# Kernel optimization log

Hardware: AMD Instinct MI355X
Metric: run time of the kernel (lower is better)

Reference implementation:

```python
import jax, jax.numpy as jnp
import numpy as np

D = 768
H = 12
HD = D // H
FF = 3072
EPS = 1e-5


def layernorm(x, g, b):
    mu = jnp.mean(x, axis=-1, keepdims=True)
    var = jnp.mean(jnp.square(x - mu), axis=-1, keepdims=True)
    return (x - mu) * jax.lax.rsqrt(var + EPS) * g + b


def setup_inputs() -> dict:
    key = jax.random.key(0)
    ks = jax.random.split(key, 12)
    s = 0.02
    return {
        "x": jax.random.normal(ks[0], (4, 1024, D), dtype=jnp.float32),
        "w_qkv": jax.random.normal(ks[1], (D, 3 * D), dtype=jnp.float32) * s,
        "b_qkv": jnp.zeros((3 * D,), jnp.float32),
        "w_proj": jax.random.normal(ks[2], (D, D), dtype=jnp.float32) * s,
        "b_proj": jnp.zeros((D,), jnp.float32),
        "w1": jax.random.normal(ks[3], (D, FF), dtype=jnp.float32) * s,
        "b1": jnp.zeros((FF,), jnp.float32),
        "w2": jax.random.normal(ks[4], (FF, D), dtype=jnp.float32) * s,
        "b2": jnp.zeros((D,), jnp.float32),
        "g1": jnp.ones((D,), jnp.float32),
        "be1": jnp.zeros((D,), jnp.float32),
        "g2": jnp.ones((D,), jnp.float32),
        "be2": jnp.zeros((D,), jnp.float32),
    }


def reference(x, w_qkv, b_qkv, w_proj, b_proj, w1, b1, w2, b2, g1, be1, g2, be2):
    B, N, C = x.shape
    # --- attention (pre-norm) ---
    h = layernorm(x, g1, be1)
    qkv = (h @ w_qkv + b_qkv).reshape(B, N, 3, H, HD)
    q = jnp.transpose(qkv[:, :, 0], (0, 2, 1, 3))  # [B,H,N,hd]
    k = jnp.transpose(qkv[:, :, 1], (0, 2, 1, 3))
    v = jnp.transpose(qkv[:, :, 2], (0, 2, 1, 3))
    attn = jnp.einsum("bhqd,bhkd->bhqk", q, k) * (HD ** -0.5)
    attn = jax.nn.softmax(attn, axis=-1)
    o = jnp.einsum("bhqk,bhkd->bhqd", attn, v)
    o = jnp.transpose(o, (0, 2, 1, 3)).reshape(B, N, C)
    x = x + (o @ w_proj + b_proj)
    # --- feedforward (pre-norm) ---
    h2 = layernorm(x, g2, be2)
    ff = jax.nn.gelu(h2 @ w1 + b1, approximate=False) @ w2 + b2
    return x + ff
```

## Files before the change

### kernel.cpp

```cpp
#include <hip/hip_runtime.h>
#include <hip/hip_bf16.h>
#include <math.h>

typedef __attribute__((ext_vector_type(8))) short short8;
typedef __attribute__((ext_vector_type(4))) float f32x4;

#define DMODEL 768
#define THREE_D 2304
#define FFDIM 3072
#define NSEQ 1024
#define NHEAD 12
#define HEADD 64
#define MROWS 4096

__device__ __forceinline__ ushort f2bf(float f) {
  union { float f; unsigned u; } c; c.f = f;
  unsigned u = c.u;
  unsigned r = (u + 0x7fffu + ((u >> 16) & 1u)) >> 16;
  return (ushort)r;
}

__device__ __forceinline__ float bf2f(ushort u) {
  union { float f; unsigned u; } c; c.u = ((unsigned)u) << 16; return c.f;
}

__device__ __forceinline__ unsigned pack2bf(float a, float b) {
  union { __hip_bfloat162 h; unsigned u; } c;
  c.h = __float22bfloat162_rn(make_float2(a, b));
  return c.u;
}

__device__ __forceinline__ void load_lds16(const ushort* g, const ushort* l) {
  __builtin_amdgcn_global_load_lds(
      (const __attribute__((address_space(1))) unsigned int*)g,
      (__attribute__((address_space(3))) unsigned int*)l, 16, 0, 0);
}

template <int N> __device__ __forceinline__ void wait_vm() {
  if constexpr (N == 8)      asm volatile("s_waitcnt vmcnt(8)" ::: "memory");
  else if constexpr (N == 6) asm volatile("s_waitcnt vmcnt(6)" ::: "memory");
  else if constexpr (N == 4) asm volatile("s_waitcnt vmcnt(4)" ::: "memory");
  else                       asm volatile("s_waitcnt vmcnt(0)" ::: "memory");
}

__device__ __forceinline__ void ln_body(const float* __restrict__ x,
    const float* __restrict__ g, const float* __restrict__ be,
    ushort* __restrict__ out, int row, int tid,
    float* red1, float* red2) {
  const float* xr = x + (size_t)row * DMODEL;
  float v0 = xr[tid], v1 = xr[tid + 256], v2 = xr[tid + 512];
  float s = v0 + v1 + v2;
  #pragma unroll
  for (int off = 32; off; off >>= 1) s += __shfl_xor(s, off);
  if ((tid & 63) == 0) red1[tid >> 6] = s;
  __syncthreads();
  float mean = (red1[0] + red1[1] + red1[2] + red1[3]) * (1.0f / 768.0f);
  float d0 = v0 - mean, d1 = v1 - mean, d2 = v2 - mean;
  float q = d0 * d0 + d1 * d1 + d2 * d2;
  #pragma unroll
  for (int off = 32; off; off >>= 1) q += __shfl_xor(q, off);
  if ((tid & 63) == 0) red2[tid >> 6] = q;
  __syncthreads();
  float var = (red2[0] + red2[1] + red2[2] + red2[3]) * (1.0f / 768.0f);
  float rs = rsqrtf(var + 1e-5f);
  size_t base = (size_t)row * DMODEL;
  out[base + tid]       = f2bf(d0 * rs * g[tid]       + be[tid]);
  out[base + tid + 256] = f2bf(d1 * rs * g[tid + 256] + be[tid + 256]);
  out[base + tid + 512] = f2bf(d2 * rs * g[tid + 512] + be[tid + 512]);
}

__global__ __launch_bounds__(256) void ln_bf16_kernel(
    const ushort* __restrict__ x, const float* __restrict__ g,
    const float* __restrict__ be, ushort* __restrict__ out) {
  __shared__ float red1[4], red2[4];
  int row = blockIdx.x, tid = threadIdx.x;
  const ushort* xr = x + (size_t)row * DMODEL;
  float v0 = 0.f, v1 = 0.f, v2 = 0.f, v3 = 0.f;
  if (tid < 192) {
    ushort4 u = *(const ushort4*)&xr[tid * 4];
    v0 = bf2f(u.x); v1 = bf2f(u.y); v2 = bf2f(u.z); v3 = bf2f(u.w);
  }
  float s = v0 + v1 + v2 + v3;
  #pragma unroll
  for (int off = 32; off; off >>= 1) s += __shfl_xor(s, off);
  if ((tid & 63) == 0) red1[tid >> 6] = s;
  __syncthreads();
  float mean = (red1[0] + red1[1] + red1[2] + red1[3]) * (1.0f / 768.0f);
  float d0 = v0 - mean, d1 = v1 - mean, d2 = v2 - mean, d3 = v3 - mean;
  float q = (tid < 192) ? d0 * d0 + d1 * d1 + d2 * d2 + d3 * d3 : 0.f;
  #pragma unroll
  for (int off = 32; off; off >>= 1) q += __shfl_xor(q, off);
  if ((tid & 63) == 0) red2[tid >> 6] = q;
  __syncthreads();
  float var = (red2[0] + red2[1] + red2[2] + red2[3]) * (1.0f / 768.0f);
  float rs = rsqrtf(var + 1e-5f);
  if (tid < 192) {
    int c = tid * 4;
    float o0 = d0 * rs * g[c] + be[c];
    float o1 = d1 * rs * g[c + 1] + be[c + 1];
    float o2 = d2 * rs * g[c + 2] + be[c + 2];
    float o3 = d3 * rs * g[c + 3] + be[c + 3];
    uint2 pw = make_uint2(pack2bf(o0, o1), pack2bf(o2, o3));
    *(uint2*)&out[(size_t)row * DMODEL + c] = pw;
  }
}

__global__ __launch_bounds__(256) void pre_kernel(
    const float* __restrict__ w_qkv, const float* __restrict__ w_proj,
    const float* __restrict__ w1, const float* __restrict__ w2,
    ushort* __restrict__ Wqkv_t, ushort* __restrict__ Wproj_t,
    ushort* __restrict__ W1_t, ushort* __restrict__ W2_t,
    const float* __restrict__ x, const float* __restrict__ g1,
    const float* __restrict__ be1, ushort* __restrict__ hbuf) {
  __shared__ float t[64][33];
  int id = blockIdx.x;
  int tid = threadIdx.x;
  if (id >= 3456) {
    ln_body(x, g1, be1, hbuf, id - 3456, tid, &t[0][0], &t[1][0]);
    return;
  }
  const float* W; ushort* Wt; int K, N, bx, by;
  if (id < 864)       { W = w_qkv;  Wt = Wqkv_t;  K = 768;  N = 2304; bx = id % 72; by = id / 72; }
  else if (id < 1152) { id -= 864;  W = w_proj; Wt = Wproj_t; K = 768;  N = 768;  bx = id % 24; by = id / 24; }
  else if (id < 2304) { id -= 1152; W = w1;     Wt = W1_t;    K = 768;  N = 3072; bx = id % 96; by = id / 96; }
  else                { id -= 2304; W = w2;     Wt = W2_t;    K = 3072; N = 768;  bx = id % 24; by = id / 24; }
  int n0 = bx * 32, k0 = by * 64;
  #pragma unroll
  for (int i = 0; i < 2; i++) {
    int s = tid + i * 256;
    int k = s >> 3, nq = (s & 7) * 4;
    float4 w = *(const float4*)&W[(size_t)(k0 + k) * N + n0 + nq];
    t[k][nq] = w.x; t[k][nq + 1] = w.y; t[k][nq + 2] = w.z; t[k][nq + 3] = w.w;
  }
  __syncthreads();
  {
    int n = tid >> 3, kq = (tid & 7) * 8;
    ushort u[8];
    #pragma unroll
    for (int j = 0; j < 8; j++) u[j] = f2bf(t[kq + j][n]);
    *(int4*)&Wt[(size_t)(n0 + n) * K + k0 + kq] = *(int4*)u;
  }
}

__global__ void vt_kernel(const ushort* __restrict__ qkv, ushort* __restrict__ Vt) {
  __shared__ ushort t[32][33];
  int n0 = blockIdx.x * 32, d0 = blockIdx.y * 32, bh = blockIdx.z;
  int b = bh / NHEAD, hh = bh % NHEAD;
  int tx = threadIdx.x, ty = threadIdx.y;
  #pragma unroll
  for (int r = 0; r < 4; r++)
    t[ty + r * 8][tx] = qkv[(size_t)(b * NSEQ + n0 + ty + r * 8) * THREE_D +
                            2 * DMODEL + hh * HEADD + d0 + tx];
  __syncthreads();
  #pragma unroll
  for (int r = 0; r < 4; r++) {
    int n = n0 + tx;
    int np = (n & ~63) | (((n & 15) << 2) | ((n >> 4) & 3));
    Vt[((size_t)bh * HEADD + d0 + ty + r * 8) * NSEQ + np] = t[tx][ty + r * 8];
  }
}

template <int BN, int MODE>
__global__ __launch_bounds__(512, 2) void gemm256_kernel(
    const ushort* __restrict__ A, const ushort* __restrict__ Bt,
    const float* __restrict__ bias, void* __restrict__ Cout,
    int gx, int Ntot, int K) {
  constexpr int FN = BN / 64;
  constexpr int WN = BN / 4;
  constexpr int ABUF = (256 + BN) * 64;
  constexpr int BOFF = 256 * 64;
  __shared__ ushort S[2 * ABUF];
  int tid = threadIdx.x, lane = tid & 63, wave = tid >> 6;
  int wm = wave >> 2, wn = wave & 3;
  int rsel = lane & 15, quad = lane >> 4;
  int nwg = gridDim.x;
  int o = blockIdx.x;
  int wg = (o & 7) * (nwg >> 3) + (o >> 3);
  int bx = wg % gx, by = wg / gx;
  int m0 = by * 256, n0 = bx * BN;
  f32x4 acc[8][FN] = {};
  int xorc = (rsel & 7) * 8;

  auto SA = [&](int buf, int k0, int i) {
    int c0 = i * 512 + wave * 64;
    int c = c0 + lane, r = c >> 3;
    int kk = ((c ^ r) & 7) * 8;
    load_lds16(&A[(size_t)(m0 + r) * K + k0 + kk], S + buf * ABUF + c0 * 8);
  };
  auto SB = [&](int buf, int k0, int i) {
    int c0 = i * 512 + wave * 64;
    int c = c0 + lane, r = c >> 3;
    int kk = ((c ^ r) & 7) * 8;
    load_lds16(&Bt[(size_t)(n0 + r) * K + k0 + kk],
               S + buf * ABUF + BOFF + c0 * 8);
  };
  auto RDA = [&](int cur, int half, int ks, int mi) -> short8 {
    int R = wm * 128 + (half * 4 + mi) * 16 + rsel;
    return *(const short8*)&S[cur * ABUF + R * 64 + ((ks * 32 + quad * 8) ^ xorc)];
  };
  auto RDB = [&](int cur, int ks, int ni) -> short8 {
    int R = wn * WN + ni * 16 + rsel;
    return *(const short8*)&S[cur * ABUF + BOFF + R * 64 +
                              ((ks * 32 + quad * 8) ^ xorc)];
  };

  #pragma unroll
  for (int i = 0; i < 4; i++) SA(0, 0, i);
  #pragma unroll
  for (int i = 0; i < FN; i++) SB(0, 0, i);
  wait_vm<0>();
  __builtin_amdgcn_s_barrier();

  int ntk = K >> 6;
  for (int t = 0; t < ntk; t++) {
    int cur = t & 1, nxt = cur ^ 1;
    bool pre = (t + 1 < ntk);
    int nk0 = (t + 1) * 64;
    short8 afb[2][4], bfb[2][FN];
    #pragma unroll
    for (int mi = 0; mi < 4; mi++) afb[0][mi] = RDA(cur, 0, 0, mi);
    #pragma unroll
    for (int ni = 0; ni < FN; ni++) bfb[0][ni] = RDB(cur, 0, ni);
    #pragma unroll
    for (int p = 0; p < 4; p++) {
      const int ks = p >> 1, half = p & 1;
      if (p < 3) {
        const int ksn = (p + 1) >> 1, halfn = (p + 1) & 1;
        #pragma unroll
        for (int mi = 0; mi < 4; mi++)
          afb[(p + 1) & 1][mi] = RDA(cur, halfn, ksn, mi);
        if (p == 1) {
          #pragma unroll
          for (int ni = 0; ni < FN; ni++) bfb[1][ni] = RDB(cur, 1, ni);
        }
      }
      if (pre) {
        if (p == 0) {
          #pragma unroll
          for (int i = 0; i < FN; i++) SB(nxt, nk0, i);
          SA(nxt, nk0, 0);
        } else if (p == 1) {
          SA(nxt, nk0, 1); SA(nxt, nk0, 2); SA(nxt, nk0, 3);
        }
      }
      __builtin_amdgcn_s_setprio(1);
      #pragma unroll
      for (int mi = 0; mi < 4; mi++)
        #pragma unroll
        for (int ni = 0; ni < FN; ni++)
          acc[half * 4 + mi][ni] = __builtin_amdgcn_mfma_f32_16x16x32_bf16(
              afb[p & 1][mi], bfb[ks][ni], acc[half * 4 + mi][ni], 0, 0, 0);
      __builtin_amdgcn_s_setprio(0);
    }
    wait_vm<0>();
    __builtin_amdgcn_s_barrier();
  }
  ushort* Cl = S;
  float bv[FN];
  #pragma unroll
  for (int ni = 0; ni < FN; ni++) bv[ni] = bias[n0 + wn * WN + ni * 16 + rsel];
  #pragma unroll
  for (int mi = 0; mi < 8; mi++) {
    int row = wm * 128 + mi * 16 + quad * 4;
    #pragma unroll
    for (int ni = 0; ni < FN; ni++) {
      int col = wn * WN + ni * 16 + rsel;
      #pragma unroll
      for (int j = 0; j < 4; j++) {
        float v = acc[mi][ni][j] + bv[ni];
        if (MODE == 2) v = 0.5f * v * (1.0f + erff(v * 0.70710678118654752f));
        Cl[(row + j) * 200 + col] = f2bf(v);
      }
    }
  }
  __syncthreads();
  constexpr int CPR = BN / 8;
  ushort* Cg = (ushort*)Cout;
  for (int c = tid; c < 256 * CPR; c += 512) {
    int row = c / CPR, off = c - row * CPR;
    int4 v = *(const int4*)&Cl[row * 200 + off * 8];
    *(int4*)&Cg[(size_t)(m0 + row) * Ntot + n0 + off * 8] = v;
  }
}

template <int BM, int BN, int MODE>
__global__ __launch_bounds__(256) void gemm_kernel(
    const ushort* __restrict__ A, const ushort* __restrict__ Bt,
    const float* __restrict__ bias, const void* __restrict__ resid,
    void* __restrict__ Cout, int gx, int Ntot, int K) {
  constexpr int ABUF = (BM + BN) * 64;
  constexpr int BOFF = BM * 64;
  constexpr int CSTR = BN + 4;
  constexpr int SMEM = (2 * ABUF * 2 > BM * CSTR * 4) ? 2 * ABUF
                                                      : BM * CSTR * 2;
  __shared__ ushort S[SMEM];
  constexpr int WM = BM / 2, WN = BN / 2;
  constexpr int FM = WM / 16, FN = WN / 16;
  constexpr int NL = BM / 32 + BN / 32;
  int tid = threadIdx.x, lane = tid & 63, wave = tid >> 6;
  int wm = wave >> 1, wn = wave & 1;
  int rsel = lane & 15, quad = lane >> 4;
  int nwg = gridDim.x;
  int o = blockIdx.x;
  int wg = (o & 7) * (nwg >> 3) + (o >> 3);
  int bx = wg % gx, by = wg / gx;
  int m0 = by * BM, n0 = bx * BN;
  f32x4 acc[FM][FN] = {};

  auto STAGE = [&](int buf, int k0) {
    #pragma unroll
    for (int i = 0; i < BM / 32; i++) {
      int c0 = i * 256 + wave * 64;
      int c = c0 + lane, r = c >> 3;
      int kk = ((c ^ r) & 7) * 8;
      load_lds16(&A[(size_t)(m0 + r) * K + k0 + kk], S + buf * ABUF + c0 * 8);
    }
    #pragma unroll
    for (int i = 0; i < BN / 32; i++) {
      int c0 = i * 256 + wave * 64;
      int c = c0 + lane, r = c >> 3;
      int kk = ((c ^ r) & 7) * 8;
      load_lds16(&Bt[(size_t)(n0 + r) * K + k0 + kk],
                 S + buf * ABUF + BOFF + c0 * 8);
    }
  };

  STAGE(0, 0);
  int ntk = K >> 6;
  for (int t = 0; t < ntk; t++) {
    int cur = t & 1;
    if (t + 1 < ntk) {
      STAGE(cur ^ 1, (t + 1) * 64);
      wait_vm<NL>();
    } else {
      wait_vm<0>();
    }
    __builtin_amdgcn_s_barrier();
    short8 af[2][FM], bf[2][FN];
    #pragma unroll
    for (int ks = 0; ks < 2; ks++) {
      int ko = ks * 32 + quad * 8;
      #pragma unroll
      for (int mi = 0; mi < FM; mi++) {
        int R = wm * WM + mi * 16 + rsel;
        af[ks][mi] = *(const short8*)&S[cur * ABUF + R * 64 + (ko ^ ((R & 7) * 8))];
      }
      #pragma unroll
      for (int ni = 0; ni < FN; ni++) {
        int R = wn * WN + ni * 16 + rsel;
        bf[ks][ni] = *(const short8*)&S[cur * ABUF + BOFF + R * 64 + (ko ^ ((R & 7) * 8))];
      }
    }
    #pragma unroll
    for (int ks = 0; ks < 2; ks++)
      #pragma unroll
      for (int mi = 0; mi < FM; mi++)
        #pragma unroll
        for (int ni = 0; ni < FN; ni++)
          acc[mi][ni] = __builtin_amdgcn_mfma_f32_16x16x32_bf16(
              af[ks][mi], bf[ks][ni], acc[mi][ni], 0, 0, 0);
    asm volatile("s_waitcnt lgkmcnt(0)" ::: "memory");
    __builtin_amdgcn_s_barrier();
  }
  float* Cl = (float*)S;
  #pragma unroll
  for (int ni = 0; ni < FN; ni++) {
    int col = wn * WN + ni * 16 + rsel;
    float bvv = bias[n0 + col];
    #pragma unroll
    for (int mi = 0; mi < FM; mi++) {
      int row = wm * WM + mi * 16 + quad * 4;
      #pragma unroll
      for (int j = 0; j < 4; j++)
        Cl[(row + j) * CSTR + col] = acc[mi][ni][j] + bvv;
    }
  }
  __syncthreads();
  constexpr int CPR = BN / 4;
  for (int c = tid; c < BM * CPR; c += 256) {
    int row = c / CPR, off = c - row * CPR;
    size_t gi = (size_t)(m0 + row) * Ntot + n0 + off * 4;
    float4 v = *(const float4*)&Cl[row * CSTR + off * 4];
    if (MODE == 0) {
      float4 rr = *(const float4*)&((const float*)resid)[gi];
      v.x += rr.x; v.y += rr.y; v.z += rr.z; v.w += rr.w;
      uint2 pw = make_uint2(pack2bf(v.x, v.y), pack2bf(v.z, v.w));
      *(uint2*)&((ushort*)Cout)[gi] = pw;
    } else {
      ushort4 rr = *(const ushort4*)&((const ushort*)resid)[gi];
      v.x += bf2f(rr.x); v.y += bf2f(rr.y);
      v.z += bf2f(rr.z); v.w += bf2f(rr.w);
      *(float4*)&((float*)Cout)[gi] = v;
    }
  }
}

__global__ __launch_bounds__(512) void attn_kernel(
    const ushort* __restrict__ qkv, const ushort* __restrict__ Vt,
    ushort* __restrict__ o) {
  __shared__ ushort Klds[2][64][64];
  __shared__ ushort Vlds[2][64][64];
  __shared__ ushort Plds[8][16][72];
  const float CL2 = 0.18033688011112042f;
  int tid = threadIdx.x, lane = tid & 63, wave = tid >> 6;
  int id = blockIdx.x;
  int qt = id / 48, bh = id % 48;
  int b = bh / NHEAD, hh = bh % NHEAD;
  int q0 = qt * 128;
  int rsel = lane & 15, quad = lane >> 4;
  int xorc = (rsel & 7) * 8;

  short8 qf[2];
  {
    int qrow = q0 + wave * 16 + rsel;
    const ushort* qp = qkv + (size_t)(b * NSEQ + qrow) * THREE_D + hh * HEADD + quad * 8;
    qf[0] = *(const short8*)qp;
    qf[1] = *(const short8*)(qp + 32);
  }
  short8 onesf;
  #pragma unroll
  for (int i = 0; i < 8; i++) onesf[i] = (short)0x3F80;

  int r0 = tid >> 3, d0 = (tid & 7) * 8;
  int sw0 = d0 ^ ((r0 & 7) * 8);
  const ushort* Kg = qkv + (size_t)b * NSEQ * THREE_D + DMODEL + hh * HEADD;
  const ushort* Vg = Vt + (size_t)bh * HEADD * NSEQ;
  int4 kr0, vr0;
  auto LD = [&](int kv0) {
    kr0 = *(const int4*)&Kg[(size_t)(kv0 + r0) * THREE_D + d0];
    vr0 = *(const int4*)&Vg[(size_t)r0 * NSEQ + kv0 + d0];
  };
  auto ST = [&](int bf) {
    *(int4*)&Klds[bf][r0][sw0] = kr0;
    *(int4*)&Vlds[bf][r0][sw0] = vr0;
  };

  f32x4 oacc[4] = {};
  f32x4 osum = {};

  LD(0); ST(0); __syncthreads();

  for (int t = 0; t < 16; t++) {
    int bf = t & 1;
    if (t < 15) LD((t + 1) * 64);
    f32x4 sfr[4] = {};
    __builtin_amdgcn_s_setprio(1);
    #pragma unroll
    for (int ks = 0; ks < 2; ks++) {
      int ko = ks * 32 + quad * 8;
      #pragma unroll
      for (int nt = 0; nt < 4; nt++) {
        short8 kf = *(const short8*)&Klds[bf][nt * 16 + rsel][ko ^ xorc];
        sfr[nt] = __builtin_amdgcn_mfma_f32_16x16x32_bf16(qf[ks], kf, sfr[nt], 0, 0, 0);
      }
    }
    __builtin_amdgcn_s_setprio(0);
    #pragma unroll
    for (int i = 0; i < 4; i++) {
      float p0 = exp2f(fmaf(sfr[0][i], CL2, -12.0f));
      float p1 = exp2f(fmaf(sfr[1][i], CL2, -12.0f));
      float p2 = exp2f(fmaf(sfr[2][i], CL2, -12.0f));
      float p3 = exp2f(fmaf(sfr[3][i], CL2, -12.0f));
      uint2 pw = make_uint2(pack2bf(p0, p1), pack2bf(p2, p3));
      *(uint2*)&Plds[wave][quad * 4 + i][rsel * 4] = pw;
    }
    __builtin_amdgcn_s_setprio(1);
    #pragma unroll
    for (int ks = 0; ks < 2; ks++) {
      int ko = ks * 32 + quad * 8;
      short8 pf = *(const short8*)&Plds[wave][rsel][ko];
      #pragma unroll
      for (int nt = 0; nt < 4; nt++) {
        short8 vf = *(const short8*)&Vlds[bf][nt * 16 + rsel][ko ^ xorc];
        oacc[nt] = __builtin_amdgcn_mfma_f32_16x16x32_bf16(pf, vf, oacc[nt], 0, 0, 0);
      }
      osum = __builtin_amdgcn_mfma_f32_16x16x32_bf16(pf, onesf, osum, 0, 0, 0);
    }
    __builtin_amdgcn_s_setprio(0);
    if (t < 15) ST(bf ^ 1);
    __syncthreads();
  }
  float rin[4];
  #pragma unroll
  for (int i = 0; i < 4; i++) rin[i] = __builtin_amdgcn_rcpf(osum[i]);
  #pragma unroll
  for (int nt = 0; nt < 4; nt++)
    #pragma unroll
    for (int i = 0; i < 4; i++) {
      int qrow = q0 + wave * 16 + quad * 4 + i;
      int col = hh * HEADD + nt * 16 + rsel;
      o[(size_t)(b * NSEQ + qrow) * DMODEL + col] = f2bf(oacc[nt][i] * rin[i]);
    }
}

extern "C" void kernel_launch(void* const* d_in, const int* in_sizes, int n_in,
                              void* d_out, int out_size, void* d_ws, size_t ws_size,
                              hipStream_t stream) {
  const float* x      = (const float*)d_in[0];
  const float* w_qkv  = (const float*)d_in[1];
  const float* b_qkv  = (const float*)d_in[2];
  const float* w_proj = (const float*)d_in[3];
  const float* b_proj = (const float*)d_in[4];
  const float* w1     = (const float*)d_in[5];
  const float* b1     = (const float*)d_in[6];
  const float* w2     = (const float*)d_in[7];
  const float* b2     = (const float*)d_in[8];
  const float* g1     = (const float*)d_in[9];
  const float* be1    = (const float*)d_in[10];
  const float* g2     = (const float*)d_in[11];
  const float* be2    = (const float*)d_in[12];
  float* out = (float*)d_out;

  char* ws = (char*)d_ws;
  ushort* Wqkv_t  = (ushort*)(ws + 0);
  ushort* Wproj_t = (ushort*)(ws + 3538944);
  ushort* W1_t    = (ushort*)(ws + 4718592);
  ushort* W2_t    = (ushort*)(ws + 9437184);
  ushort* hbuf    = (ushort*)(ws + 14155776);
  ushort* qkv     = (ushort*)(ws + 20447232);
  ushort* ff1     = qkv;
  ushort* VtB     = (ushort*)(ws + 45613056);
  ushort* obuf    = (ushort*)(ws + 51904512);
  ushort* x2      = (ushort*)(ws + 58195968);

  dim3 tb(32, 8);
  pre_kernel<<<3456 + 4096, 256, 0, stream>>>(
      w_qkv, w_proj, w1, w2, Wqkv_t, Wproj_t, W1_t, W2_t,
      x, g1, be1, hbuf);

  gemm256_kernel<192, 0><<<192, 512, 0, stream>>>(
      hbuf, Wqkv_t, b_qkv, qkv, THREE_D / 192, THREE_D, DMODEL);

  vt_kernel<<<dim3(NSEQ / 32, HEADD / 32, 4 * NHEAD), tb, 0, stream>>>(qkv, VtB);

  attn_kernel<<<384, 512, 0, stream>>>(qkv, VtB, obuf);

  gemm_kernel<128, 64, 0><<<384, 256, 0, stream>>>(
      obuf, Wproj_t, b_proj, x, x2, DMODEL / 64, DMODEL, DMODEL);

  ln_bf16_kernel<<<MROWS, 256, 0, stream>>>(x2, g2, be2, hbuf);

  gemm256_kernel<192, 2><<<256, 512, 0, stream>>>(
      hbuf, W1_t, b1, ff1, FFDIM / 192, FFDIM, DMODEL);

  gemm_kernel<128, 64, 1><<<384, 256, 0, stream>>>(
      ff1, W2_t, b2, x2, out, DMODEL / 64, DMODEL, FFDIM);

  (void)in_sizes; (void)n_in; (void)out_size; (void)ws_size;
}
```

Baseline: 150.7 us.

## Fuse V transpose into QKV GEMM epilogue and use 8-wave 128x64 GEMM tiles

The separate vt_kernel is removed. The QKV GEMM epilogue now writes the permuted, transposed V directly from its LDS tile for blocks covering the V columns, which saves a launch and a re-read of V from global memory. The 128x64 projection and FF2 GEMMs now run with 512 threads (8 waves, each computing a 32x32 sub-tile) instead of 256, to raise per-block parallelism and latency hiding. The cost is more waves per block sharing the same LDS tile and extra scattered 4-byte global stores in the QKV epilogue.

New measurement: 145.9 us. 3.2% less time.

```diff
diff --git a/kernel.cpp b/kernel.cpp
--- a/kernel.cpp
+++ b/kernel.cpp
@@ -40,6 +40,7 @@
   if constexpr (N == 8)      asm volatile("s_waitcnt vmcnt(8)" ::: "memory");
   else if constexpr (N == 6) asm volatile("s_waitcnt vmcnt(6)" ::: "memory");
   else if constexpr (N == 4) asm volatile("s_waitcnt vmcnt(4)" ::: "memory");
+  else if constexpr (N == 3) asm volatile("s_waitcnt vmcnt(3)" ::: "memory");
   else                       asm volatile("s_waitcnt vmcnt(0)" ::: "memory");
 }
 
@@ -142,29 +143,11 @@
   }
 }
 
-__global__ void vt_kernel(const ushort* __restrict__ qkv, ushort* __restrict__ Vt) {
-  __shared__ ushort t[32][33];
-  int n0 = blockIdx.x * 32, d0 = blockIdx.y * 32, bh = blockIdx.z;
-  int b = bh / NHEAD, hh = bh % NHEAD;
-  int tx = threadIdx.x, ty = threadIdx.y;
-  #pragma unroll
-  for (int r = 0; r < 4; r++)
-    t[ty + r * 8][tx] = qkv[(size_t)(b * NSEQ + n0 + ty + r * 8) * THREE_D +
-                            2 * DMODEL + hh * HEADD + d0 + tx];
-  __syncthreads();
-  #pragma unroll
-  for (int r = 0; r < 4; r++) {
-    int n = n0 + tx;
-    int np = (n & ~63) | (((n & 15) << 2) | ((n >> 4) & 3));
-    Vt[((size_t)bh * HEADD + d0 + ty + r * 8) * NSEQ + np] = t[tx][ty + r * 8];
-  }
-}
-
-template <int BN, int MODE>
+template <int BN, int MODE, bool VOUT>
 __global__ __launch_bounds__(512, 2) void gemm256_kernel(
     const ushort* __restrict__ A, const ushort* __restrict__ Bt,
     const float* __restrict__ bias, void* __restrict__ Cout,
-    int gx, int Ntot, int K) {
+    ushort* __restrict__ Vt, int gx, int Ntot, int K) {
   constexpr int FN = BN / 64;
   constexpr int WN = BN / 4;
   constexpr int ABUF = (256 + BN) * 64;
@@ -281,10 +264,26 @@
     int4 v = *(const int4*)&Cl[row * 200 + off * 8];
     *(int4*)&Cg[(size_t)(m0 + row) * Ntot + n0 + off * 8] = v;
   }
+  if (VOUT && n0 >= 2 * DMODEL) {
+    int b = m0 >> 10, nsb = m0 & 1023;
+    int np2 = (tid & 127) * 2;
+    int t64 = np2 & ~63;
+    int o1 = np2 & 63;
+    int r1 = t64 + (((o1 & 3) << 4) | (o1 >> 2));
+    int r2 = t64 + ((((o1 + 1) & 3) << 4) | ((o1 + 1) >> 2));
+    for (int cb = tid >> 7; cb < BN; cb += 4) {
+      int n = n0 + cb - 2 * DMODEL;
+      int hh = n >> 6, d = n & 63;
+      unsigned pw = (unsigned)Cl[r1 * 200 + cb] |
+                    ((unsigned)Cl[r2 * 200 + cb] << 16);
+      *(unsigned*)&Vt[(((size_t)(b * NHEAD + hh) * HEADD + d) * NSEQ) +
+                      nsb + np2] = pw;
+    }
+  }
 }
 
 template <int BM, int BN, int MODE>
-__global__ __launch_bounds__(256) void gemm_kernel(
+__global__ __launch_bounds__(512) void gemm_kernel(
     const ushort* __restrict__ A, const ushort* __restrict__ Bt,
     const float* __restrict__ bias, const void* __restrict__ resid,
     void* __restrict__ Cout, int gx, int Ntot, int K) {
@@ -294,9 +293,6 @@
   constexpr int SMEM = (2 * ABUF * 2 > BM * CSTR * 4) ? 2 * ABUF
                                                       : BM * CSTR * 2;
   __shared__ ushort S[SMEM];
-  constexpr int WM = BM / 2, WN = BN / 2;
-  constexpr int FM = WM / 16, FN = WN / 16;
-  constexpr int NL = BM / 32 + BN / 32;
   int tid = threadIdx.x, lane = tid & 63, wave = tid >> 6;
   int wm = wave >> 1, wn = wave & 1;
   int rsel = lane & 15, quad = lane >> 4;
@@ -305,19 +301,18 @@
   int wg = (o & 7) * (nwg >> 3) + (o >> 3);
   int bx = wg % gx, by = wg / gx;
   int m0 = by * BM, n0 = bx * BN;
-  f32x4 acc[FM][FN] = {};
+  f32x4 acc[2][2] = {};
 
   auto STAGE = [&](int buf, int k0) {
     #pragma unroll
-    for (int i = 0; i < BM / 32; i++) {
-      int c0 = i * 256 + wave * 64;
+    for (int i = 0; i < BM / 64; i++) {
+      int c0 = i * 512 + wave * 64;
       int c = c0 + lane, r = c >> 3;
       int kk = ((c ^ r) & 7) * 8;
       load_lds16(&A[(size_t)(m0 + r) * K + k0 + kk], S + buf * ABUF + c0 * 8);
     }
-    #pragma unroll
-    for (int i = 0; i < BN / 32; i++) {
-      int c0 = i * 256 + wave * 64;
+    {
+      int c0 = wave * 64;
       int c = c0 + lane, r = c >> 3;
       int kk = ((c ^ r) & 7) * 8;
       load_lds16(&Bt[(size_t)(n0 + r) * K + k0 + kk],
@@ -331,32 +326,32 @@
     int cur = t & 1;
     if (t + 1 < ntk) {
       STAGE(cur ^ 1, (t + 1) * 64);
-      wait_vm<NL>();
+      wait_vm<3>();
     } else {
       wait_vm<0>();
     }
     __builtin_amdgcn_s_barrier();
-    short8 af[2][FM], bf[2][FN];
+    short8 af[2][2], bf[2][2];
     #pragma unroll
     for (int ks = 0; ks < 2; ks++) {
       int ko = ks * 32 + quad * 8;
       #pragma unroll
-      for (int mi = 0; mi < FM; mi++) {
-        int R = wm * WM + mi * 16 + rsel;
+      for (int mi = 0; mi < 2; mi++) {
+        int R = wm * 32 + mi * 16 + rsel;
         af[ks][mi] = *(const short8*)&S[cur * ABUF + R * 64 + (ko ^ ((R & 7) * 8))];
       }
       #pragma unroll
-      for (int ni = 0; ni < FN; ni++) {
-        int R = wn * WN + ni * 16 + rsel;
+      for (int ni = 0; ni < 2; ni++) {
+        int R = wn * 32 + ni * 16 + rsel;
         bf[ks][ni] = *(const short8*)&S[cur * ABUF + BOFF + R * 64 + (ko ^ ((R & 7) * 8))];
       }
     }
     #pragma unroll
     for (int ks = 0; ks < 2; ks++)
       #pragma unroll
-      for (int mi = 0; mi < FM; mi++)
+      for (int mi = 0; mi < 2; mi++)
         #pragma unroll
-        for (int ni = 0; ni < FN; ni++)
+        for (int ni = 0; ni < 2; ni++)
           acc[mi][ni] = __builtin_amdgcn_mfma_f32_16x16x32_bf16(
               af[ks][mi], bf[ks][ni], acc[mi][ni], 0, 0, 0);
     asm volatile("s_waitcnt lgkmcnt(0)" ::: "memory");
@@ -364,12 +359,12 @@
   }
   float* Cl = (float*)S;
   #pragma unroll
-  for (int ni = 0; ni < FN; ni++) {
-    int col = wn * WN + ni * 16 + rsel;
+  for (int ni = 0; ni < 2; ni++) {
+    int col = wn * 32 + ni * 16 + rsel;
     float bvv = bias[n0 + col];
     #pragma unroll
-    for (int mi = 0; mi < FM; mi++) {
-      int row = wm * WM + mi * 16 + quad * 4;
+    for (int mi = 0; mi < 2; mi++) {
+      int row = wm * 32 + mi * 16 + quad * 4;
       #pragma unroll
       for (int j = 0; j < 4; j++)
         Cl[(row + j) * CSTR + col] = acc[mi][ni][j] + bvv;
@@ -377,7 +372,7 @@
   }
   __syncthreads();
   constexpr int CPR = BN / 4;
-  for (int c = tid; c < BM * CPR; c += 256) {
+  for (int c = tid; c < BM * CPR; c += 512) {
     int row = c / CPR, off = c - row * CPR;
     size_t gi = (size_t)(m0 + row) * Ntot + n0 + off * 4;
     float4 v = *(const float4*)&Cl[row * CSTR + off * 4];
@@ -523,27 +518,24 @@
   ushort* obuf    = (ushort*)(ws + 51904512);
   ushort* x2      = (ushort*)(ws + 58195968);
 
-  dim3 tb(32, 8);
   pre_kernel<<<3456 + 4096, 256, 0, stream>>>(
       w_qkv, w_proj, w1, w2, Wqkv_t, Wproj_t, W1_t, W2_t,
       x, g1, be1, hbuf);
 
-  gemm256_kernel<192, 0><<<192, 512, 0, stream>>>(
-      hbuf, Wqkv_t, b_qkv, qkv, THREE_D / 192, THREE_D, DMODEL);
-
-  vt_kernel<<<dim3(NSEQ / 32, HEADD / 32, 4 * NHEAD), tb, 0, stream>>>(qkv, VtB);
+  gemm256_kernel<192, 0, true><<<192, 512, 0, stream>>>(
+      hbuf, Wqkv_t, b_qkv, qkv, VtB, THREE_D / 192, THREE_D, DMODEL);
 
   attn_kernel<<<384, 512, 0, stream>>>(qkv, VtB, obuf);
 
-  gemm_kernel<128, 64, 0><<<384, 256, 0, stream>>>(
+  gemm_kernel<128, 64, 0><<<384, 512, 0, stream>>>(
       obuf, Wproj_t, b_proj, x, x2, DMODEL / 64, DMODEL, DMODEL);
 
   ln_bf16_kernel<<<MROWS, 256, 0, stream>>>(x2, g2, be2, hbuf);
 
-  gemm256_kernel<192, 2><<<256, 512, 0, stream>>>(
-      hbuf, W1_t, b1, ff1, FFDIM / 192, FFDIM, DMODEL);
-
-  gemm_kernel<128, 64, 1><<<384, 256, 0, stream>>>(
+  gemm256_kernel<192, 2, false><<<256, 512, 0, stream>>>(
+      hbuf, W1_t, b1, ff1, nullptr, FFDIM / 192, FFDIM, DMODEL);
+
+  gemm_kernel<128, 64, 1><<<384, 512, 0, stream>>>(
       ff1, W2_t, b2, x2, out, DMODEL / 64, DMODEL, FFDIM);
 
   (void)in_sizes; (void)n_in; (void)out_size; (void)ws_size;
```
